# Performance work log

Hardware: AMD Instinct MI355X
Metric: run time of the kernel (lower is better)

Reference implementation:

```python
import jax, jax.numpy as jnp
import numpy as np

D_MODEL = 1024
N_HEADS = 16
DIM_HEAD = 64
NUM_MEM_KV = 16
INNER = N_HEADS * DIM_HEAD  # 1024


def setup_inputs() -> dict:
    key = jax.random.key(0)
    ks = jax.random.split(key, 8)
    s = 0.02
    x = jax.random.normal(ks[0], (2, 2048, D_MODEL), dtype=jnp.float32)
    Wq = jax.random.normal(ks[1], (D_MODEL, INNER), dtype=jnp.float32) * s
    Wkv = jax.random.normal(ks[2], (D_MODEL, 2 * INNER), dtype=jnp.float32) * s
    Wo = jax.random.normal(ks[3], (INNER, D_MODEL), dtype=jnp.float32) * s
    pre_proj = jax.random.normal(ks[4], (N_HEADS, N_HEADS), dtype=jnp.float32)
    post_proj = jax.random.normal(ks[5], (N_HEADS, N_HEADS), dtype=jnp.float32)
    mem_k = jax.random.normal(ks[6], (N_HEADS, NUM_MEM_KV, DIM_HEAD), dtype=jnp.float32)
    mem_v = jax.random.normal(ks[7], (N_HEADS, NUM_MEM_KV, DIM_HEAD), dtype=jnp.float32)
    return {"x": x, "Wq": Wq, "Wkv": Wkv, "Wo": Wo,
            "pre_proj": pre_proj, "post_proj": post_proj,
            "mem_k": mem_k, "mem_v": mem_v}


def reference(x, Wq, Wkv, Wo, pre_proj, post_proj, mem_k, mem_v):
    b, n, _ = x.shape
    scale = DIM_HEAD ** -0.5
    # projections (no bias)
    q = x @ Wq                              # [b, n, inner]
    kv = x @ Wkv                            # self-attention: context = x
    k, v = jnp.split(kv, 2, axis=-1)
    split_heads = lambda t: t.reshape(b, n, N_HEADS, DIM_HEAD).transpose(0, 2, 1, 3)
    q, k, v = split_heads(q), split_heads(k), split_heads(v)  # [b, h, n, d]
    # prepend memory key/values along kv axis
    mk = jnp.broadcast_to(mem_k[None], (b, N_HEADS, NUM_MEM_KV, DIM_HEAD))
    mv = jnp.broadcast_to(mem_v[None], (b, N_HEADS, NUM_MEM_KV, DIM_HEAD))
    k = jnp.concatenate([mk, k], axis=2)    # [b, h, j, d], j = mem + n
    v = jnp.concatenate([mv, v], axis=2)
    dots = jnp.einsum('bhid,bhjd->bhij', q, k) * scale
    # pre-softmax talking-heads mixing
    dots = jnp.einsum('bhij,hk->bkij', dots, pre_proj)
    # causal mask with mem-kv offset: triu(ones(i,j), j-i+1)
    i, j = dots.shape[-2], dots.shape[-1]
    causal = jnp.triu(jnp.ones((i, j), dtype=bool), k=j - i + 1)
    mask_value = jnp.finfo(dots.dtype).min
    dots = jnp.where(causal[None, None], mask_value, dots)
    attn = jax.nn.softmax(dots, axis=-1)
    # post-softmax talking-heads mixing
    attn = jnp.einsum('bhij,hk->bkij', attn, post_proj)
    out = jnp.einsum('bhij,bhjd->bhid', attn, v)   # [b, h, n, d]
    out = out.transpose(0, 2, 1, 3).reshape(b, n, INNER)
    return out @ Wo                                # [b, n, d_model]
```

## Files before the change

kernel.cpp:

```cpp
#include <hip/hip_runtime.h>


typedef __attribute__((ext_vector_type(8))) short short8;
typedef __attribute__((ext_vector_type(4))) float floatx4;

#define MFMA16(a, b, c) __builtin_amdgcn_mfma_f32_16x16x32_bf16(a, b, c, 0, 0, 0)
#define BARLDS() __asm__ volatile("s_waitcnt lgkmcnt(0)\n\ts_barrier" ::: "memory")
#define LGKM0() __asm__ volatile("s_waitcnt lgkmcnt(0)" ::: "memory")

static __device__ __forceinline__ unsigned short f2bf(float f) {
  union { float f; unsigned u; } v; v.f = f;
  unsigned r = v.u + 0x7fffu + ((v.u >> 16) & 1u);
  return (unsigned short)(r >> 16);
}
static __device__ __forceinline__ float bf2f(unsigned short h) {
  union { unsigned u; float f; } v; v.u = ((unsigned)h) << 16;
  return v.f;
}

union S8U { short8 v; unsigned short u[8]; };

__global__ __launch_bounds__(256) void conv_bf16(const float* __restrict__ src,
                                                 unsigned short* __restrict__ dst,
                                                 int n8) {
  int tid = blockIdx.x * 256 + threadIdx.x;
  if (tid >= n8) return;
  const float4* s = (const float4*)src + (size_t)tid * 2;
  float4 a = s[0], b = s[1];
  S8U o;
  o.u[0] = f2bf(a.x); o.u[1] = f2bf(a.y); o.u[2] = f2bf(a.z); o.u[3] = f2bf(a.w);
  o.u[4] = f2bf(b.x); o.u[5] = f2bf(b.y); o.u[6] = f2bf(b.z); o.u[7] = f2bf(b.w);
  *(short8*)(dst + (size_t)tid * 8) = o.v;
}

__global__ __launch_bounds__(256) void transW(const float* __restrict__ src, int Ncols,
                                              unsigned short* __restrict__ dst, int dstRowOff) {
  __shared__ float sw[32][33];
  int n0 = blockIdx.x * 32, k0 = blockIdx.y * 32;
  int t = threadIdx.x;
  int lk = t >> 3, n4 = (t & 7) * 4;
  const float* s = src + (size_t)(k0 + lk) * Ncols + n0 + n4;
  sw[lk][n4 + 0] = s[0]; sw[lk][n4 + 1] = s[1];
  sw[lk][n4 + 2] = s[2]; sw[lk][n4 + 3] = s[3];
  __syncthreads();
  int ln = t >> 3, k4 = (t & 7) * 4;
  unsigned o0 = f2bf(sw[k4 + 0][ln]) | ((unsigned)f2bf(sw[k4 + 1][ln]) << 16);
  unsigned o1 = f2bf(sw[k4 + 2][ln]) | ((unsigned)f2bf(sw[k4 + 3][ln]) << 16);
  uint2 pk; pk.x = o0; pk.y = o1;
  *(uint2*)(dst + (size_t)(dstRowOff + n0 + ln) * 1024 + k0 + k4) = pk;
}

__global__ __launch_bounds__(256) void gemm_bt(const unsigned short* __restrict__ A,
                                               const unsigned short* __restrict__ BT,
                                               unsigned short* __restrict__ Cb,
                                               float* __restrict__ Cf,
                                               int M, int N, int K, int f32out) {
  int w = threadIdx.x >> 6, lane = threadIdx.x & 63;
  int quad = lane >> 4, l16 = lane & 15;
  int m0 = blockIdx.x * 128 + (w >> 1) * 64;
  int n0 = blockIdx.y * 128 + (w & 1) * 64;
  floatx4 acc[4][4];
#pragma unroll
  for (int i = 0; i < 4; i++)
#pragma unroll
    for (int j = 0; j < 4; j++) acc[i][j] = (floatx4){0.f, 0.f, 0.f, 0.f};

  for (int kk = 0; kk < K; kk += 32) {
    short8 af[4], bf[4];
#pragma unroll
    for (int t = 0; t < 4; t++) {
      af[t] = *(const short8*)(A + (size_t)(m0 + t * 16 + l16) * K + kk + quad * 8);
      bf[t] = *(const short8*)(BT + (size_t)(n0 + t * 16 + l16) * K + kk + quad * 8);
    }
#pragma unroll
    for (int mt = 0; mt < 4; mt++)
#pragma unroll
      for (int nt = 0; nt < 4; nt++) acc[mt][nt] = MFMA16(af[mt], bf[nt], acc[mt][nt]);
  }
#pragma unroll
  for (int mt = 0; mt < 4; mt++)
#pragma unroll
    for (int nt = 0; nt < 4; nt++)
#pragma unroll
      for (int r = 0; r < 4; r++) {
        size_t row = m0 + mt * 16 + quad * 4 + r;
        size_t col = n0 + nt * 16 + l16;
        if (f32out) Cf[row * N + col] = acc[mt][nt][r];
        else Cb[row * N + col] = f2bf(acc[mt][nt][r]);
      }
}

__global__ __launch_bounds__(256) void fill_K(const unsigned short* __restrict__ qkv,
                                              const float* __restrict__ mem_k,
                                              unsigned short* __restrict__ Kw) {
  int tid = blockIdx.x * 256 + threadIdx.x;
  if (tid >= 2 * 16 * 2064 * 8) return;
  int d0 = (tid & 7) * 8;
  int j = (tid >> 3) % 2064;
  int h = ((tid >> 3) / 2064) & 15;
  int b = (tid >> 3) / (2064 * 16);
  S8U o;
  if (j < 16) {
    const float* s = mem_k + ((size_t)(h * 16 + j) * 64 + d0);
#pragma unroll
    for (int c = 0; c < 8; c++) o.u[c] = f2bf(s[c]);
  } else {
    o.v = *(const short8*)(qkv + (size_t)(b * 2048 + j - 16) * 3072 + 1024 + h * 64 + d0);
  }
  *(short8*)(Kw + ((size_t)(b * 16 + h) * 2064 + j) * 64 + d0) = o.v;
}

__global__ __launch_bounds__(256) void fill_Vt(const unsigned short* __restrict__ qkv,
                                               const float* __restrict__ mem_v,
                                               unsigned short* __restrict__ Vt) {
  __shared__ float sv[16][65];
  int jt = blockIdx.x, h = blockIdx.y, b = blockIdx.z;
  int t = threadIdx.x;
  int j = t >> 4, d0 = (t & 15) * 4;
  int jg = jt * 16 + j;
  float v0, v1, v2, v3;
  if (jg < 16) {
    const float* s = mem_v + ((size_t)(h * 16 + jg) * 64 + d0);
    v0 = s[0]; v1 = s[1]; v2 = s[2]; v3 = s[3];
  } else {
    const unsigned short* s = qkv + (size_t)(b * 2048 + jg - 16) * 3072 + 2048 + h * 64 + d0;
    v0 = bf2f(s[0]); v1 = bf2f(s[1]); v2 = bf2f(s[2]); v3 = bf2f(s[3]);
  }
  sv[j][d0 + 0] = v0; sv[j][d0 + 1] = v1; sv[j][d0 + 2] = v2; sv[j][d0 + 3] = v3;
  __syncthreads();
  int d = t >> 2, j4 = (t & 3) * 4;
  unsigned o0 = f2bf(sv[j4 + 0][d]) | ((unsigned)f2bf(sv[j4 + 1][d]) << 16);
  unsigned o1 = f2bf(sv[j4 + 2][d]) | ((unsigned)f2bf(sv[j4 + 3][d]) << 16);
  uint2 pk; pk.x = o0; pk.y = o1;
  *(uint2*)(Vt + ((size_t)(b * 16 + h) * 64 + d) * 2064 + jt * 16 + j4) = pk;
}

__global__ __launch_bounds__(1024) void attn_stats(const unsigned short* __restrict__ qkv,
                                                   const unsigned short* __restrict__ Kw,
                                                   const float* __restrict__ pre,
                                                   float* __restrict__ l_ws) {
  const int c = blockIdx.x, it = blockIdx.y, b = blockIdx.z;
  const int i0 = it * 64;
  const int jmax = i0 + 80;
  const int jc0 = c * 160;
  if (jc0 >= jmax) return;
  const int jend = min(jmax, jc0 + 160);
  const int niter = (jend - jc0 + 31) >> 5;

  __shared__ unsigned short S_lds[64 * 776];

  const int tid = threadIdx.x, w = tid >> 6, lane = tid & 63;
  const int quad = lane >> 4, l16 = lane & 15;
  const int hoff = (quad < 2) ? quad * 8 : 0;

  short8 qa[4][2];
#pragma unroll
  for (int s = 0; s < 4; s++) {
    const unsigned short* p =
        qkv + (size_t)(b * 2048 + i0 + s * 16 + l16) * 3072 + w * 64 + quad * 8;
    qa[s][0] = *(const short8*)p;
    qa[s][1] = *(const short8*)(p + 32);
  }
  short8 preA;
#pragma unroll
  for (int jj = 0; jj < 8; jj++) {
    int h = quad * 8 + jj;
    preA[jj] = (short)((quad < 2) ? f2bf(pre[h * 16 + l16] * 0.125f) : 0);
  }
  const unsigned short* Kb = Kw + (size_t)(b * 16 + w) * 2064 * 64;

  float l_loc[4][4];
#pragma unroll
  for (int i4 = 0; i4 < 4; i4++)
#pragma unroll
    for (int r = 0; r < 4; r++) l_loc[i4][r] = 0.f;

  short8 kf[2][2];
#pragma unroll
  for (int jt = 0; jt < 2; jt++) {
    int jr = min(jc0 + jt * 16 + l16, 2063);
    const unsigned short* kp = Kb + (size_t)jr * 64 + quad * 8;
    kf[jt][0] = *(const short8*)kp;
    kf[jt][1] = *(const short8*)(kp + 32);
  }

  for (int n = 0; n < niter; n++) {
    const int j0 = jc0 + n * 32;
#pragma unroll
    for (int jt = 0; jt < 2; jt++)
#pragma unroll
      for (int s = 0; s < 4; s++) {
        floatx4 a = (floatx4){0.f, 0.f, 0.f, 0.f};
        a = MFMA16(qa[s][0], kf[jt][0], a);
        a = MFMA16(qa[s][1], kf[jt][1], a);
#pragma unroll
        for (int r = 0; r < 4; r++)
          S_lds[(s * 16 + quad * 4 + r) * 776 + (jt * 16 + l16) * 24 + w] = f2bf(a[r]);
      }
    if (n + 1 < niter) {
      const int j0n = j0 + 32;
#pragma unroll
      for (int jt = 0; jt < 2; jt++) {
        int jr = min(j0n + jt * 16 + l16, 2063);
        const unsigned short* kp = Kb + (size_t)jr * 64 + quad * 8;
        kf[jt][0] = *(const short8*)kp;
        kf[jt][1] = *(const short8*)(kp + 32);
      }
    }
    BARLDS();
#pragma unroll
    for (int u = 0; u < 8; u++) {
      const int iloc = u >> 1, jt = u & 1, ii = w * 4 + iloc;
      const short8 bb = *(const short8*)(S_lds + ii * 776 + (jt * 16 + l16) * 24 + hoff);
      floatx4 sp = (floatx4){0.f, 0.f, 0.f, 0.f};
      sp = MFMA16(preA, bb, sp);
      const int jg = j0 + jt * 16 + l16;
      if (jg <= i0 + ii + 16) {
#pragma unroll
        for (int r = 0; r < 4; r++) l_loc[iloc][r] += __expf(sp[r]);
      }
    }
    BARLDS();
  }
#pragma unroll
  for (int iloc = 0; iloc < 4; iloc++)
#pragma unroll
    for (int r = 0; r < 4; r++) {
      float v = l_loc[iloc][r];
      v += __shfl_xor(v, 1);
      v += __shfl_xor(v, 2);
      v += __shfl_xor(v, 4);
      v += __shfl_xor(v, 8);
      if (l16 == 0)
        atomicAdd(l_ws + ((size_t)(b * 2048 + i0 + w * 4 + iloc) * 16 + quad * 4 + r), v);
    }
}

__global__ __launch_bounds__(1024) void attn_av(const unsigned short* __restrict__ qkv,
                                                const unsigned short* __restrict__ Kw,
                                                const unsigned short* __restrict__ Vt,
                                                const float* __restrict__ pre,
                                                const float* __restrict__ post,
                                                const float* __restrict__ l_ws,
                                                float* __restrict__ O_ws) {
  const int c = blockIdx.x, it = blockIdx.y, b = blockIdx.z;
  const int i0 = it * 32;
  const int jmax = i0 + 48;
  const int jc0 = c * 160;
  if (jc0 >= jmax) return;
  const int jend = min(jmax, jc0 + 160);
  const int niter = (jend - jc0 + 31) >> 5;

  __shared__ unsigned short S_lds[32 * 776];
  __shared__ unsigned short Pp_lds[16 * 1288];

  const int tid = threadIdx.x, w = tid >> 6, lane = tid & 63;
  const int quad = lane >> 4, l16 = lane & 15;
  const int hoff = (quad < 2) ? quad * 8 : 0;

  short8 qa[2][2];
#pragma unroll
  for (int s = 0; s < 2; s++) {
    const unsigned short* p =
        qkv + (size_t)(b * 2048 + i0 + s * 16 + l16) * 3072 + w * 64 + quad * 8;
    qa[s][0] = *(const short8*)p;
    qa[s][1] = *(const short8*)(p + 32);
  }
  short8 preA, postA;
#pragma unroll
  for (int jj = 0; jj < 8; jj++) {
    int h = quad * 8 + jj;
    float pv = 0.f, qv = 0.f;
    if (quad < 2) { pv = pre[h * 16 + l16] * 0.125f; qv = post[h * 16 + l16]; }
    preA[jj] = (short)f2bf(pv);
    postA[jj] = (short)f2bf(qv);
  }
  float rl[2][4];
#pragma unroll
  for (int iloc = 0; iloc < 2; iloc++)
#pragma unroll
    for (int r = 0; r < 4; r++)
      rl[iloc][r] = 1.0f / l_ws[(size_t)(b * 2048 + i0 + w * 2 + iloc) * 16 + quad * 4 + r];

  floatx4 oacc[2][4];
#pragma unroll
  for (int g = 0; g < 2; g++)
#pragma unroll
    for (int d = 0; d < 4; d++) oacc[g][d] = (floatx4){0.f, 0.f, 0.f, 0.f};

  const unsigned short* Kb = Kw + (size_t)(b * 16 + w) * 2064 * 64;
  const unsigned short* Vb = Vt + (size_t)(b * 16 + w) * 64 * 2064;

  short8 kf[2][2];
#pragma unroll
  for (int jt = 0; jt < 2; jt++) {
    int jr = min(jc0 + jt * 16 + l16, 2063);
    const unsigned short* kp = Kb + (size_t)jr * 64 + quad * 8;
    kf[jt][0] = *(const short8*)kp;
    kf[jt][1] = *(const short8*)(kp + 32);
  }

  for (int n = 0; n < niter; n++) {
    const int j0 = jc0 + n * 32;
    short8 vf[4];
    {
      const int jc = min(j0 + quad * 8, 2056);
#pragma unroll
      for (int d = 0; d < 4; d++)
        vf[d] = *(const short8*)(Vb + (size_t)(d * 16 + l16) * 2064 + jc);
    }
#pragma unroll
    for (int jt = 0; jt < 2; jt++)
#pragma unroll
      for (int s = 0; s < 2; s++) {
        floatx4 a = (floatx4){0.f, 0.f, 0.f, 0.f};
        a = MFMA16(qa[s][0], kf[jt][0], a);
        a = MFMA16(qa[s][1], kf[jt][1], a);
#pragma unroll
        for (int r = 0; r < 4; r++)
          S_lds[(s * 16 + quad * 4 + r) * 776 + (jt * 16 + l16) * 24 + w] = f2bf(a[r]);
      }
    if (n + 1 < niter) {
      const int j0n = j0 + 32;
#pragma unroll
      for (int jt = 0; jt < 2; jt++) {
        int jr = min(j0n + jt * 16 + l16, 2063);
        const unsigned short* kp = Kb + (size_t)jr * 64 + quad * 8;
        kf[jt][0] = *(const short8*)kp;
        kf[jt][1] = *(const short8*)(kp + 32);
      }
    }
    BARLDS();
#pragma unroll
    for (int u = 0; u < 4; u++) {
      const int iloc = u >> 1, jt = u & 1, ii = w * 2 + iloc;
      const int sc = ii * 776 + (jt * 16 + l16) * 24;
      const short8 bb = *(const short8*)(S_lds + sc + hoff);
      floatx4 sp = (floatx4){0.f, 0.f, 0.f, 0.f};
      sp = MFMA16(preA, bb, sp);
      const int jg = j0 + jt * 16 + l16;
      const bool keep = jg <= (i0 + ii + 16);
#pragma unroll
      for (int r = 0; r < 4; r++)
        S_lds[sc + quad * 4 + r] = f2bf(keep ? __expf(sp[r]) * rl[iloc][r] : 0.f);
    }
    LGKM0();
#pragma unroll
    for (int u = 0; u < 4; u++) {
      const int iloc = u >> 1, jt = u & 1, ii = w * 2 + iloc;
      const int sc = ii * 776 + (jt * 16 + l16) * 24;
      const short8 pf = *(const short8*)(S_lds + sc + hoff);
      floatx4 pp = (floatx4){0.f, 0.f, 0.f, 0.f};
      pp = MFMA16(postA, pf, pp);
#pragma unroll
      for (int r = 0; r < 4; r++)
        Pp_lds[(quad * 4 + r) * 1288 + ii * 40 + jt * 16 + l16] = f2bf(pp[r]);
    }
    BARLDS();
#pragma unroll
    for (int g = 0; g < 2; g++) {
      const short8 paf = *(const short8*)(Pp_lds + w * 1288 + (g * 16 + l16) * 40 + quad * 8);
#pragma unroll
      for (int d = 0; d < 4; d++) oacc[g][d] = MFMA16(paf, vf[d], oacc[g][d]);
    }
  }
#pragma unroll
  for (int g = 0; g < 2; g++)
#pragma unroll
    for (int d = 0; d < 4; d++)
#pragma unroll
      for (int r = 0; r < 4; r++)
        atomicAdd(O_ws + (size_t)(b * 2048 + i0 + g * 16 + quad * 4 + r) * 1024 +
                      w * 64 + d * 16 + l16,
                  oacc[g][d][r]);
}

extern "C" void kernel_launch(void* const* d_in, const int* in_sizes, int n_in,
                              void* d_out, int out_size, void* d_ws, size_t ws_size,
                              hipStream_t stream) {
  (void)in_sizes; (void)n_in; (void)out_size; (void)ws_size;
  const float* x     = (const float*)d_in[0];
  const float* Wq    = (const float*)d_in[1];
  const float* Wkv   = (const float*)d_in[2];
  const float* Wo    = (const float*)d_in[3];
  const float* pre   = (const float*)d_in[4];
  const float* post  = (const float*)d_in[5];
  const float* mem_k = (const float*)d_in[6];
  const float* mem_v = (const float*)d_in[7];
  float* out = (float*)d_out;
  char* ws = (char*)d_ws;

  unsigned short* xb     = (unsigned short*)(ws);
  unsigned short* WbT    = (unsigned short*)(ws + 8388608);
  float*          O_ws   = (float*)(ws);
  unsigned short* qkv    = (unsigned short*)(ws + 16777216);
  unsigned short* WoT    = (unsigned short*)(ws + 16777216);
  unsigned short* Kw     = (unsigned short*)(ws + 41943040);
  unsigned short* Vt     = (unsigned short*)(ws + 50397184);
  float*          l_ws   = (float*)(ws + 58851328);
  unsigned short* attn_b = (unsigned short*)(ws + 58851328);

  conv_bf16<<<2048, 256, 0, stream>>>(x, xb, 524288);
  transW<<<dim3(32, 32), 256, 0, stream>>>(Wq, 1024, WbT, 0);
  transW<<<dim3(64, 32), 256, 0, stream>>>(Wkv, 2048, WbT, 1024);
  gemm_bt<<<dim3(32, 24), 256, 0, stream>>>(xb, WbT, qkv, nullptr, 4096, 3072, 1024, 0);
  fill_K<<<2064, 256, 0, stream>>>(qkv, mem_k, Kw);
  fill_Vt<<<dim3(129, 16, 2), 256, 0, stream>>>(qkv, mem_v, Vt);
  hipMemsetAsync(O_ws, 0, 16777216, stream);
  hipMemsetAsync(l_ws, 0, 262144, stream);
  attn_stats<<<dim3(13, 32, 2), 1024, 0, stream>>>(qkv, Kw, pre, l_ws);
  attn_av<<<dim3(13, 64, 2), 1024, 0, stream>>>(qkv, Kw, Vt, pre, post, l_ws, O_ws);
  conv_bf16<<<2048, 256, 0, stream>>>(O_ws, attn_b, 524288);
  transW<<<dim3(32, 32), 256, 0, stream>>>(Wo, 1024, WoT, 0);
  gemm_bt<<<dim3(32, 8), 256, 0, stream>>>(attn_b, WoT, nullptr, out, 4096, 1024, 1024, 1);
}
```

Measured before the change: 487.1 us.

## Double-buffer LDS and software-pipeline QK/mix/AV stages in attention kernels

Both attention kernels now use ping-pong LDS buffers and double-buffered K/V register fragments. The QK MFMA for the next chunk, and its global loads, are issued while the current chunk's head-mixing and softmax run, which removes one barrier per iteration. Query tiles are halved (32 rows for stats, 16 for AV) and the grid is flattened so that chunk index varies slowest, giving more and smaller blocks. In exchange, K loads are repeated across twice as many query tiles and there are twice as many atomic adds to the outputs.

```diff
diff --git a/kernel.cpp b/kernel.cpp
--- a/kernel.cpp
+++ b/kernel.cpp
@@ -135,27 +135,69 @@
   *(uint2*)(Vt + ((size_t)(b * 16 + h) * 64 + d) * 2064 + jt * 16 + j4) = pk;
 }
 
+
+#define ST_LOADK(KF, J0)                                                      \
+  { _Pragma("unroll") for (int jt = 0; jt < 2; jt++) {                        \
+      int jr = min((J0) + jt * 16 + l16, 2063);                               \
+      const unsigned short* kp = Kb + (size_t)jr * 64 + quad * 8;             \
+      KF[jt][0] = *(const short8*)kp;                                         \
+      KF[jt][1] = *(const short8*)(kp + 32);                                  \
+  } }
+
+#define ST_QK(SDST, KF)                                                      \
+  { _Pragma("unroll") for (int jt = 0; jt < 2; jt++)                         \
+      _Pragma("unroll") for (int s = 0; s < 2; s++) {                        \
+        floatx4 a = (floatx4){0.f, 0.f, 0.f, 0.f};                           \
+        a = MFMA16(qa[s][0], KF[jt][0], a);                                  \
+        a = MFMA16(qa[s][1], KF[jt][1], a);                                  \
+        _Pragma("unroll") for (int r = 0; r < 4; r++)                        \
+          (SDST)[(s * 16 + quad * 4 + r) * 776 + (jt * 16 + l16) * 24 + w] = \
+              f2bf(a[r]);                                                    \
+  } }
+
+#define ST_BODY(SCUR, SOTH, KF_USE, KF_LOAD)                                 \
+  { const int j0 = jc0 + n * 32;                                             \
+    _Pragma("unroll") for (int u = 0; u < 4; u++) {                          \
+      const int iloc = u >> 1, jt = u & 1, ii = w * 2 + iloc;                \
+      const short8 bb =                                                      \
+          *(const short8*)((SCUR) + ii * 776 + (jt * 16 + l16) * 24 + hoff); \
+      floatx4 sp = (floatx4){0.f, 0.f, 0.f, 0.f};                            \
+      sp = MFMA16(preA, bb, sp);                                             \
+      const int jg = j0 + jt * 16 + l16;                                     \
+      if (jg <= i0 + ii + 16) {                                              \
+        _Pragma("unroll") for (int r = 0; r < 4; r++)                        \
+          l_loc[iloc][r] += __expf(sp[r]);                                   \
+      }                                                                      \
+    }                                                                        \
+    if (n + 1 < niter) ST_QK(SOTH, KF_USE);                                  \
+    if (n + 2 < niter) ST_LOADK(KF_LOAD, jc0 + (n + 2) * 32);                \
+    if (n + 1 < niter) BARLDS();                                             \
+  }
+
 __global__ __launch_bounds__(1024) void attn_stats(const unsigned short* __restrict__ qkv,
                                                    const unsigned short* __restrict__ Kw,
                                                    const float* __restrict__ pre,
                                                    float* __restrict__ l_ws) {
-  const int c = blockIdx.x, it = blockIdx.y, b = blockIdx.z;
-  const int i0 = it * 64;
-  const int jmax = i0 + 80;
+  const int id = blockIdx.x;
+  const int c = id >> 7, g = id & 127, it = g & 63, b = g >> 6;
+  const int i0 = it * 32;
+  const int jmax = i0 + 48;
   const int jc0 = c * 160;
   if (jc0 >= jmax) return;
   const int jend = min(jmax, jc0 + 160);
   const int niter = (jend - jc0 + 31) >> 5;
 
-  __shared__ unsigned short S_lds[64 * 776];
+  __shared__ unsigned short S_lds[2][32 * 776];
 
   const int tid = threadIdx.x, w = tid >> 6, lane = tid & 63;
   const int quad = lane >> 4, l16 = lane & 15;
   const int hoff = (quad < 2) ? quad * 8 : 0;
-
-  short8 qa[4][2];
-#pragma unroll
-  for (int s = 0; s < 4; s++) {
+  unsigned short* const S0 = S_lds[0];
+  unsigned short* const S1 = S_lds[1];
+
+  short8 qa[2][2];
+#pragma unroll
+  for (int s = 0; s < 2; s++) {
     const unsigned short* p =
         qkv + (size_t)(b * 2048 + i0 + s * 16 + l16) * 3072 + w * 64 + quad * 8;
     qa[s][0] = *(const short8*)p;
@@ -169,61 +211,28 @@
   }
   const unsigned short* Kb = Kw + (size_t)(b * 16 + w) * 2064 * 64;
 
-  float l_loc[4][4];
-#pragma unroll
-  for (int i4 = 0; i4 < 4; i4++)
+  float l_loc[2][4];
+#pragma unroll
+  for (int i4 = 0; i4 < 2; i4++)
 #pragma unroll
     for (int r = 0; r < 4; r++) l_loc[i4][r] = 0.f;
 
-  short8 kf[2][2];
-#pragma unroll
-  for (int jt = 0; jt < 2; jt++) {
-    int jr = min(jc0 + jt * 16 + l16, 2063);
-    const unsigned short* kp = Kb + (size_t)jr * 64 + quad * 8;
-    kf[jt][0] = *(const short8*)kp;
-    kf[jt][1] = *(const short8*)(kp + 32);
-  }
-
-  for (int n = 0; n < niter; n++) {
-    const int j0 = jc0 + n * 32;
-#pragma unroll
-    for (int jt = 0; jt < 2; jt++)
-#pragma unroll
-      for (int s = 0; s < 4; s++) {
-        floatx4 a = (floatx4){0.f, 0.f, 0.f, 0.f};
-        a = MFMA16(qa[s][0], kf[jt][0], a);
-        a = MFMA16(qa[s][1], kf[jt][1], a);
-#pragma unroll
-        for (int r = 0; r < 4; r++)
-          S_lds[(s * 16 + quad * 4 + r) * 776 + (jt * 16 + l16) * 24 + w] = f2bf(a[r]);
-      }
-    if (n + 1 < niter) {
-      const int j0n = j0 + 32;
-#pragma unroll
-      for (int jt = 0; jt < 2; jt++) {
-        int jr = min(j0n + jt * 16 + l16, 2063);
-        const unsigned short* kp = Kb + (size_t)jr * 64 + quad * 8;
-        kf[jt][0] = *(const short8*)kp;
-        kf[jt][1] = *(const short8*)(kp + 32);
-      }
-    }
-    BARLDS();
-#pragma unroll
-    for (int u = 0; u < 8; u++) {
-      const int iloc = u >> 1, jt = u & 1, ii = w * 4 + iloc;
-      const short8 bb = *(const short8*)(S_lds + ii * 776 + (jt * 16 + l16) * 24 + hoff);
-      floatx4 sp = (floatx4){0.f, 0.f, 0.f, 0.f};
-      sp = MFMA16(preA, bb, sp);
-      const int jg = j0 + jt * 16 + l16;
-      if (jg <= i0 + ii + 16) {
-#pragma unroll
-        for (int r = 0; r < 4; r++) l_loc[iloc][r] += __expf(sp[r]);
-      }
-    }
-    BARLDS();
-  }
-#pragma unroll
-  for (int iloc = 0; iloc < 4; iloc++)
+  short8 kfA[2][2], kfB[2][2];
+  ST_LOADK(kfA, jc0);
+  ST_QK(S0, kfA);
+  if (niter > 1) ST_LOADK(kfB, jc0 + 32);
+  BARLDS();
+
+  int n = 0;
+  while (true) {
+    ST_BODY(S0, S1, kfB, kfA);
+    if (++n == niter) break;
+    ST_BODY(S1, S0, kfA, kfB);
+    if (++n == niter) break;
+  }
+
+#pragma unroll
+  for (int iloc = 0; iloc < 2; iloc++)
 #pragma unroll
     for (int r = 0; r < 4; r++) {
       float v = l_loc[iloc][r];
@@ -232,9 +241,67 @@
       v += __shfl_xor(v, 4);
       v += __shfl_xor(v, 8);
       if (l16 == 0)
-        atomicAdd(l_ws + ((size_t)(b * 2048 + i0 + w * 4 + iloc) * 16 + quad * 4 + r), v);
+        atomicAdd(l_ws + ((size_t)(b * 2048 + i0 + w * 2 + iloc) * 16 + quad * 4 + r), v);
     }
 }
+
+
+#define AV_LOADK(KF, J0)                                                      \
+  { _Pragma("unroll") for (int jt = 0; jt < 2; jt++) {                        \
+      int jr = min((J0) + jt * 16 + l16, 2063);                               \
+      const unsigned short* kp = Kb + (size_t)jr * 64 + quad * 8;             \
+      KF[jt][0] = *(const short8*)kp;                                         \
+      KF[jt][1] = *(const short8*)(kp + 32);                                  \
+  } }
+
+#define AV_LOADV(VF, J0)                                                      \
+  { const int jc = min((J0) + quad * 8, 2056);                                \
+    _Pragma("unroll") for (int d = 0; d < 4; d++)                             \
+      VF[d] = *(const short8*)(Vb + (size_t)(d * 16 + l16) * 2064 + jc); }
+
+#define AV_QK(SDST, KF)                                                      \
+  { _Pragma("unroll") for (int jt = 0; jt < 2; jt++) {                       \
+      floatx4 a = (floatx4){0.f, 0.f, 0.f, 0.f};                             \
+      a = MFMA16(qa[0], KF[jt][0], a);                                       \
+      a = MFMA16(qa[1], KF[jt][1], a);                                       \
+      _Pragma("unroll") for (int r = 0; r < 4; r++)                          \
+        (SDST)[(quad * 4 + r) * 776 + (jt * 16 + l16) * 24 + w] = f2bf(a[r]); \
+  } }
+
+#define AV_MIX(SCUR, PPDST, J0)                                              \
+  { _Pragma("unroll") for (int jt = 0; jt < 2; jt++) {                       \
+      const int sc = w * 776 + (jt * 16 + l16) * 24;                         \
+      const short8 bb = *(const short8*)((SCUR) + sc + hoff);                \
+      floatx4 sp = (floatx4){0.f, 0.f, 0.f, 0.f};                            \
+      sp = MFMA16(preA, bb, sp);                                             \
+      const int jg = (J0) + jt * 16 + l16;                                   \
+      const bool keep = jg <= i0 + w + 16;                                   \
+      _Pragma("unroll") for (int r = 0; r < 4; r++)                          \
+        (SCUR)[sc + quad * 4 + r] = f2bf(keep ? __expf(sp[r]) * rl[r] : 0.f);\
+    }                                                                        \
+    LGKM0();                   \
+    _Pragma("unroll") for (int jt = 0; jt < 2; jt++) {                       \
+      const int sc = w * 776 + (jt * 16 + l16) * 24;                         \
+      const short8 pf = *(const short8*)((SCUR) + sc + hoff);                \
+      floatx4 pp = (floatx4){0.f, 0.f, 0.f, 0.f};                            \
+      pp = MFMA16(postA, pf, pp);                                            \
+      _Pragma("unroll") for (int r = 0; r < 4; r++)                          \
+        (PPDST)[(quad * 4 + r) * 648 + w * 40 + jt * 16 + l16] = f2bf(pp[r]); \
+  } }
+
+#define AV_AV(PPSRC, VF)                                                     \
+  { const short8 paf =                                                       \
+        *(const short8*)((PPSRC) + w * 648 + l16 * 40 + quad * 8);           \
+    _Pragma("unroll") for (int d = 0; d < 4; d++)                            \
+      oacc[d] = MFMA16(paf, VF[d], oacc[d]); }
+
+#define AV_BODY(SCUR, SOTH, PPCUR, PPOTH, KFOTH, KFCUR, VFOTH)               \
+  { if (n > 0) AV_AV(PPOTH, VFOTH);                                          \
+    AV_MIX(SCUR, PPCUR, jc0 + n * 32);                                       \
+    if (n + 1 < niter) AV_QK(SOTH, KFOTH);                                   \
+    if (n + 2 < niter) AV_LOADK(KFCUR, jc0 + (n + 2) * 32);                  \
+    if (n + 1 < niter) AV_LOADV(VFOTH, jc0 + (n + 1) * 32);                  \
+    BARLDS(); }
 
 __global__ __launch_bounds__(1024) void attn_av(const unsigned short* __restrict__ qkv,
                                                 const unsigned short* __restrict__ Kw,
@@ -243,28 +310,32 @@
                                                 const float* __restrict__ post,
                                                 const float* __restrict__ l_ws,
                                                 float* __restrict__ O_ws) {
-  const int c = blockIdx.x, it = blockIdx.y, b = blockIdx.z;
-  const int i0 = it * 32;
-  const int jmax = i0 + 48;
+  const int id = blockIdx.x;
+  const int c = id >> 8, g = id & 255, it = g & 127, b = g >> 7;
+  const int i0 = it * 16;
+  const int jmax = i0 + 32;
   const int jc0 = c * 160;
   if (jc0 >= jmax) return;
   const int jend = min(jmax, jc0 + 160);
   const int niter = (jend - jc0 + 31) >> 5;
 
-  __shared__ unsigned short S_lds[32 * 776];
-  __shared__ unsigned short Pp_lds[16 * 1288];
+  __shared__ unsigned short S_lds[2][16 * 776];
+  __shared__ unsigned short Pp_lds[2][16 * 648];
 
   const int tid = threadIdx.x, w = tid >> 6, lane = tid & 63;
   const int quad = lane >> 4, l16 = lane & 15;
   const int hoff = (quad < 2) ? quad * 8 : 0;
-
-  short8 qa[2][2];
-#pragma unroll
-  for (int s = 0; s < 2; s++) {
+  unsigned short* const S0 = S_lds[0];
+  unsigned short* const S1 = S_lds[1];
+  unsigned short* const Pp0 = Pp_lds[0];
+  unsigned short* const Pp1 = Pp_lds[1];
+
+  short8 qa[2];
+  {
     const unsigned short* p =
-        qkv + (size_t)(b * 2048 + i0 + s * 16 + l16) * 3072 + w * 64 + quad * 8;
-    qa[s][0] = *(const short8*)p;
-    qa[s][1] = *(const short8*)(p + 32);
+        qkv + (size_t)(b * 2048 + i0 + l16) * 3072 + w * 64 + quad * 8;
+    qa[0] = *(const short8*)p;
+    qa[1] = *(const short8*)(p + 32);
   }
   short8 preA, postA;
 #pragma unroll
@@ -275,104 +346,41 @@
     preA[jj] = (short)f2bf(pv);
     postA[jj] = (short)f2bf(qv);
   }
-  float rl[2][4];
-#pragma unroll
-  for (int iloc = 0; iloc < 2; iloc++)
-#pragma unroll
-    for (int r = 0; r < 4; r++)
-      rl[iloc][r] = 1.0f / l_ws[(size_t)(b * 2048 + i0 + w * 2 + iloc) * 16 + quad * 4 + r];
-
-  floatx4 oacc[2][4];
-#pragma unroll
-  for (int g = 0; g < 2; g++)
-#pragma unroll
-    for (int d = 0; d < 4; d++) oacc[g][d] = (floatx4){0.f, 0.f, 0.f, 0.f};
+  float rl[4];
+#pragma unroll
+  for (int r = 0; r < 4; r++)
+    rl[r] = 1.0f / l_ws[(size_t)(b * 2048 + i0 + w) * 16 + quad * 4 + r];
+
+  floatx4 oacc[4];
+#pragma unroll
+  for (int d = 0; d < 4; d++) oacc[d] = (floatx4){0.f, 0.f, 0.f, 0.f};
 
   const unsigned short* Kb = Kw + (size_t)(b * 16 + w) * 2064 * 64;
   const unsigned short* Vb = Vt + (size_t)(b * 16 + w) * 64 * 2064;
 
-  short8 kf[2][2];
-#pragma unroll
-  for (int jt = 0; jt < 2; jt++) {
-    int jr = min(jc0 + jt * 16 + l16, 2063);
-    const unsigned short* kp = Kb + (size_t)jr * 64 + quad * 8;
-    kf[jt][0] = *(const short8*)kp;
-    kf[jt][1] = *(const short8*)(kp + 32);
-  }
-
-  for (int n = 0; n < niter; n++) {
-    const int j0 = jc0 + n * 32;
-    short8 vf[4];
-    {
-      const int jc = min(j0 + quad * 8, 2056);
-#pragma unroll
-      for (int d = 0; d < 4; d++)
-        vf[d] = *(const short8*)(Vb + (size_t)(d * 16 + l16) * 2064 + jc);
-    }
-#pragma unroll
-    for (int jt = 0; jt < 2; jt++)
-#pragma unroll
-      for (int s = 0; s < 2; s++) {
-        floatx4 a = (floatx4){0.f, 0.f, 0.f, 0.f};
-        a = MFMA16(qa[s][0], kf[jt][0], a);
-        a = MFMA16(qa[s][1], kf[jt][1], a);
-#pragma unroll
-        for (int r = 0; r < 4; r++)
-          S_lds[(s * 16 + quad * 4 + r) * 776 + (jt * 16 + l16) * 24 + w] = f2bf(a[r]);
-      }
-    if (n + 1 < niter) {
-      const int j0n = j0 + 32;
-#pragma unroll
-      for (int jt = 0; jt < 2; jt++) {
-        int jr = min(j0n + jt * 16 + l16, 2063);
-        const unsigned short* kp = Kb + (size_t)jr * 64 + quad * 8;
-        kf[jt][0] = *(const short8*)kp;
-        kf[jt][1] = *(const short8*)(kp + 32);
-      }
-    }
-    BARLDS();
-#pragma unroll
-    for (int u = 0; u < 4; u++) {
-      const int iloc = u >> 1, jt = u & 1, ii = w * 2 + iloc;
-      const int sc = ii * 776 + (jt * 16 + l16) * 24;
-      const short8 bb = *(const short8*)(S_lds + sc + hoff);
-      floatx4 sp = (floatx4){0.f, 0.f, 0.f, 0.f};
-      sp = MFMA16(preA, bb, sp);
-      const int jg = j0 + jt * 16 + l16;
-      const bool keep = jg <= (i0 + ii + 16);
-#pragma unroll
-      for (int r = 0; r < 4; r++)
-        S_lds[sc + quad * 4 + r] = f2bf(keep ? __expf(sp[r]) * rl[iloc][r] : 0.f);
-    }
-    LGKM0();
-#pragma unroll
-    for (int u = 0; u < 4; u++) {
-      const int iloc = u >> 1, jt = u & 1, ii = w * 2 + iloc;
-      const int sc = ii * 776 + (jt * 16 + l16) * 24;
-      const short8 pf = *(const short8*)(S_lds + sc + hoff);
-      floatx4 pp = (floatx4){0.f, 0.f, 0.f, 0.f};
-      pp = MFMA16(postA, pf, pp);
-#pragma unroll
-      for (int r = 0; r < 4; r++)
-        Pp_lds[(quad * 4 + r) * 1288 + ii * 40 + jt * 16 + l16] = f2bf(pp[r]);
-    }
-    BARLDS();
-#pragma unroll
-    for (int g = 0; g < 2; g++) {
-      const short8 paf = *(const short8*)(Pp_lds + w * 1288 + (g * 16 + l16) * 40 + quad * 8);
-#pragma unroll
-      for (int d = 0; d < 4; d++) oacc[g][d] = MFMA16(paf, vf[d], oacc[g][d]);
-    }
-  }
-#pragma unroll
-  for (int g = 0; g < 2; g++)
-#pragma unroll
-    for (int d = 0; d < 4; d++)
-#pragma unroll
-      for (int r = 0; r < 4; r++)
-        atomicAdd(O_ws + (size_t)(b * 2048 + i0 + g * 16 + quad * 4 + r) * 1024 +
-                      w * 64 + d * 16 + l16,
-                  oacc[g][d][r]);
+  short8 kfA[2][2], kfB[2][2];
+  short8 vfA[4], vfB[4];
+  AV_LOADV(vfA, jc0);
+  AV_LOADK(kfA, jc0);
+  AV_QK(S0, kfA);
+  if (niter > 1) AV_LOADK(kfB, jc0 + 32);
+  BARLDS();
+
+  int n = 0;
+  while (true) {
+    AV_BODY(S0, S1, Pp0, Pp1, kfB, kfA, vfB);
+    if (++n == niter) { AV_AV(Pp0, vfA); break; }
+    AV_BODY(S1, S0, Pp1, Pp0, kfA, kfB, vfA);
+    if (++n == niter) { AV_AV(Pp1, vfB); break; }
+  }
+
+#pragma unroll
+  for (int d = 0; d < 4; d++)
+#pragma unroll
+    for (int r = 0; r < 4; r++)
+      atomicAdd(O_ws + (size_t)(b * 2048 + i0 + quad * 4 + r) * 1024 +
+                    w * 64 + d * 16 + l16,
+                oacc[d][r]);
 }
 
 extern "C" void kernel_launch(void* const* d_in, const int* in_sizes, int n_in,
@@ -408,8 +416,8 @@
   fill_Vt<<<dim3(129, 16, 2), 256, 0, stream>>>(qkv, mem_v, Vt);
   hipMemsetAsync(O_ws, 0, 16777216, stream);
   hipMemsetAsync(l_ws, 0, 262144, stream);
-  attn_stats<<<dim3(13, 32, 2), 1024, 0, stream>>>(qkv, Kw, pre, l_ws);
-  attn_av<<<dim3(13, 64, 2), 1024, 0, stream>>>(qkv, Kw, Vt, pre, post, l_ws, O_ws);
+  attn_stats<<<1664, 1024, 0, stream>>>(qkv, Kw, pre, l_ws);
+  attn_av<<<3328, 1024, 0, stream>>>(qkv, Kw, Vt, pre, post, l_ws, O_ws);
   conv_bf16<<<2048, 256, 0, stream>>>(O_ws, attn_b, 524288);
   transW<<<dim3(32, 32), 256, 0, stream>>>(Wo, 1024, WoT, 0);
   gemm_bt<<<dim3(32, 8), 256, 0, stream>>>(attn_b, WoT, nullptr, out, 4096, 1024, 1024, 1);
```

Result: slower. 638.6 us (+31.1%).
